# Kernel optimization log

Measured on AMD Instinct MI355X. Metric: run time of the kernel, lower is better.

Reference implementation:

```python
import jax, jax.numpy as jnp
import numpy as np

N_NODES = 50000
N_EDGES = 800000
D = 64  # in_dim = hidden_dim = out_dim


def gcn_conv(x, edge_index, W, b, num_nodes):
    """PyG GCNConv: x' = D^{-1/2} (A + I) D^{-1/2} (x W) + b."""
    h = x @ W  # [N, out]
    # add self-loops
    loop = jnp.arange(num_nodes, dtype=edge_index.dtype)
    row = jnp.concatenate([edge_index[0], loop])  # sources j
    col = jnp.concatenate([edge_index[1], loop])  # targets i
    # symmetric normalization
    ones = jnp.ones(row.shape[0], dtype=h.dtype)
    deg = jax.ops.segment_sum(ones, col, num_segments=num_nodes)
    dinv = jnp.where(deg > 0, jax.lax.rsqrt(deg), 0.0)
    norm = dinv[row] * dinv[col]  # [E+N]
    # gather -> scale -> scatter-add
    msg = h[row] * norm[:, None]
    out = jax.ops.segment_sum(msg, col, num_segments=num_nodes)
    return out + b


def setup_inputs() -> dict:
    key = jax.random.key(0)
    k = jax.random.split(key, 6)
    x = jax.random.normal(k[0], (N_NODES, D), dtype=jnp.float32)
    edge_index = jax.random.randint(k[1], (2, N_EDGES), 0, N_NODES, dtype=jnp.int64)
    s = 1.0 / np.sqrt(D)
    W1 = jax.random.uniform(k[2], (D, D), jnp.float32, -s, s)
    b1 = jnp.zeros((D,), jnp.float32)
    W2 = jax.random.uniform(k[3], (D, D), jnp.float32, -s, s)
    b2 = jnp.zeros((D,), jnp.float32)
    return {"x": x, "edge_index": edge_index, "W1": W1, "b1": b1, "W2": W2, "b2": b2}


def reference(x, edge_index, W1, b1, W2, b2):
    h = gcn_conv(x, edge_index, W1, b1, N_NODES)
    h = jax.nn.relu(h)
    out = gcn_conv(h, edge_index, W2, b2, N_NODES)
    return out
```

## Files before the change

### kernel.cpp

```cpp
#include <hip/hip_runtime.h>
#include <hip/hip_fp16.h>

#define N_NODES 50000
#define N_EDGES 800000
#define D 64
#define RANGES 8
#define SLICES 16
#define NPB (N_NODES / RANGES)
#define I4S (N_EDGES / SLICES / 4)
#define CAPS 12
#define CAP  48

__global__ __launch_bounds__(1024)
void partition_kernel(const int* __restrict__ row, const int* __restrict__ col,
                      unsigned char* __restrict__ cnt8,
                      unsigned short* __restrict__ ebuf) {
    __shared__ int cur[NPB];
    int tid = threadIdx.x;
    int r   = blockIdx.x & (RANGES - 1);
    int s   = blockIdx.x / RANGES;
    int lo  = r * NPB;
    for (int i = tid; i < NPB; i += 1024) cur[i] = 0;
    __syncthreads();
    const int4* c4 = (const int4*)col;
    const int4* r4 = (const int4*)row;
    size_t ebase = (size_t)s * N_NODES * CAPS;
    for (int i = s * I4S + tid; i < (s + 1) * I4S; i += 1024) {
        int4 c  = c4[i];
        int4 rr = r4[i];
        int dx = c.x - lo, dy = c.y - lo, dz = c.z - lo, dw = c.w - lo;
        if ((unsigned)dx < NPB) {
            int p = atomicAdd(&cur[dx], 1);
            if (p < CAPS) ebuf[ebase + (size_t)(lo + dx) * CAPS + p] = (unsigned short)rr.x;
        }
        if ((unsigned)dy < NPB) {
            int p = atomicAdd(&cur[dy], 1);
            if (p < CAPS) ebuf[ebase + (size_t)(lo + dy) * CAPS + p] = (unsigned short)rr.y;
        }
        if ((unsigned)dz < NPB) {
            int p = atomicAdd(&cur[dz], 1);
            if (p < CAPS) ebuf[ebase + (size_t)(lo + dz) * CAPS + p] = (unsigned short)rr.z;
        }
        if ((unsigned)dw < NPB) {
            int p = atomicAdd(&cur[dw], 1);
            if (p < CAPS) ebuf[ebase + (size_t)(lo + dw) * CAPS + p] = (unsigned short)rr.w;
        }
    }
    __syncthreads();
    for (int i = tid; i < NPB; i += 1024)
        cnt8[(size_t)s * N_NODES + lo + i] = (unsigned char)min(cur[i], CAPS);
}

__global__ __launch_bounds__(256)
void compact_kernel(const unsigned char* __restrict__ cnt8,
                    const unsigned short* __restrict__ ebuf,
                    unsigned short* __restrict__ srcs,
                    float* __restrict__ dinv, int* __restrict__ cntf) {
    int tid = threadIdx.x, lane = tid & 63;
    int node = blockIdx.x * 4 + (tid >> 6);
    int c = 0;
    if (lane < SLICES) c = cnt8[(size_t)lane * N_NODES + node];
    int pin = c;
    #pragma unroll
    for (int off = 1; off < SLICES; off <<= 1) {
        int t = __shfl_up(pin, off, 64);
        if (lane >= off && lane < SLICES) pin += t;
    }
    int n = __shfl(pin, SLICES - 1, 64);
    int kk = 0, pp = 0;
    #pragma unroll
    for (int k = 0; k < SLICES; ++k) {
        int Pk = __shfl(pin, k, 64);
        if (lane >= Pk) { kk = k + 1; pp = Pk; }
    }
    unsigned short v = 0;
    if (lane < n && lane < CAP)
        v = ebuf[((size_t)kk * N_NODES + node) * CAPS + (lane - pp)];
    if (lane < CAP) srcs[(size_t)node * CAP + lane] = v;
    if (lane == 0) {
        cntf[node] = min(n, CAP);
        dinv[node] = rsqrtf((float)(n + 1));
    }
}

__global__ __launch_bounds__(256)
void gemm_kernel(const float* __restrict__ X, const float* __restrict__ W,
                 __half* __restrict__ H) {
    int tid = threadIdx.x, lane = tid & 63, wv = tid >> 6;
    float w[64];
    #pragma unroll
    for (int k = 0; k < 64; ++k) w[k] = W[k * 64 + lane];
    int node0 = blockIdx.x * 16 + wv * 4;
    #pragma unroll
    for (int r = 0; r < 4; ++r) {
        int node = node0 + r;
        float xv = X[node * 64 + lane];
        float a0 = 0.f, a1 = 0.f;
        #pragma unroll
        for (int k = 0; k < 64; k += 2) {
            a0 = fmaf(__shfl(xv, k, 64),     w[k],     a0);
            a1 = fmaf(__shfl(xv, k + 1, 64), w[k + 1], a1);
        }
        H[node * 64 + lane] = __float2half(a0 + a1);
    }
}

template<int FUSE>
__global__ __launch_bounds__(256)
void gather_kernel(const __half* __restrict__ H, const int* __restrict__ cnt,
                   const unsigned short* __restrict__ srcs,
                   const float* __restrict__ dinv,
                   const float* __restrict__ bias, const float* __restrict__ W2,
                   void* __restrict__ outp) {
    int tid = threadIdx.x, lane = tid & 63;
    int node = blockIdx.x * 4 + (tid >> 6);
    int n = cnt[node];
    float di = dinv[node];
    const unsigned short* sp = srcs + (size_t)node * CAP;
    int s = 0; float w = 0.f;
    if (lane < n) { s = sp[lane]; w = dinv[s]; }
    float acc0 = di * __half2float(H[node * 64 + lane]);
    float acc1 = 0.f, acc2 = 0.f, acc3 = 0.f;
    int nr = (n + 7) & ~7;
    for (int j = 0; j < nr; j += 8) {
        int   s0 = __shfl(s, j + 0, 64), s1 = __shfl(s, j + 1, 64);
        int   s2 = __shfl(s, j + 2, 64), s3 = __shfl(s, j + 3, 64);
        int   s4 = __shfl(s, j + 4, 64), s5 = __shfl(s, j + 5, 64);
        int   s6 = __shfl(s, j + 6, 64), s7 = __shfl(s, j + 7, 64);
        float w0 = __shfl(w, j + 0, 64), w1 = __shfl(w, j + 1, 64);
        float w2 = __shfl(w, j + 2, 64), w3 = __shfl(w, j + 3, 64);
        float w4 = __shfl(w, j + 4, 64), w5 = __shfl(w, j + 5, 64);
        float w6 = __shfl(w, j + 6, 64), w7 = __shfl(w, j + 7, 64);
        float v0 = __half2float(H[s0 * 64 + lane]);
        float v1 = __half2float(H[s1 * 64 + lane]);
        float v2 = __half2float(H[s2 * 64 + lane]);
        float v3 = __half2float(H[s3 * 64 + lane]);
        float v4 = __half2float(H[s4 * 64 + lane]);
        float v5 = __half2float(H[s5 * 64 + lane]);
        float v6 = __half2float(H[s6 * 64 + lane]);
        float v7 = __half2float(H[s7 * 64 + lane]);
        acc0 += w0 * v0 + w4 * v4;
        acc1 += w1 * v1 + w5 * v5;
        acc2 += w2 * v2 + w6 * v6;
        acc3 += w3 * v3 + w7 * v7;
    }
    float gval = di * ((acc0 + acc1) + (acc2 + acc3)) + bias[lane];
    if constexpr (FUSE) {
        gval = fmaxf(gval, 0.f);
        float wc[64];
        #pragma unroll
        for (int k = 0; k < 64; ++k) wc[k] = W2[k * 64 + lane];
        float o0 = 0.f, o1 = 0.f;
        #pragma unroll
        for (int k = 0; k < 64; k += 2) {
            o0 = fmaf(__shfl(gval, k, 64),     wc[k],     o0);
            o1 = fmaf(__shfl(gval, k + 1, 64), wc[k + 1], o1);
        }
        ((__half*)outp)[node * 64 + lane] = __float2half(o0 + o1);
    } else {
        ((float*)outp)[node * 64 + lane] = gval;
    }
}

extern "C" void kernel_launch(void* const* d_in, const int* in_sizes, int n_in,
                              void* d_out, int out_size, void* d_ws, size_t ws_size,
                              hipStream_t stream) {
    const float* x   = (const float*)d_in[0];
    const int*   ei  = (const int*)d_in[1];
    const int*   row = ei;
    const int*   col = ei + N_EDGES;
    const float* W1  = (const float*)d_in[2];
    const float* b1  = (const float*)d_in[3];
    const float* W2  = (const float*)d_in[4];
    const float* b2  = (const float*)d_in[5];
    float* out = (float*)d_out;

    char* p = (char*)d_ws;
    __half* h = (__half*)p;            p += (size_t)N_NODES * D * 2;
    char* A = p;                       p += 20000000;
    unsigned short* ebuf = (unsigned short*)A;
    unsigned char*  cnt8 = (unsigned char*)(A + 19200000);
    __half* h2 = (__half*)A;
    unsigned short* srcs = (unsigned short*)p; p += (size_t)N_NODES * CAP * 2;
    float* dinv = (float*)p;           p += (size_t)N_NODES * 4;
    int*   cntf = (int*)p;             p += (size_t)N_NODES * 4;

    partition_kernel<<<RANGES * SLICES, 1024, 0, stream>>>(row, col, cnt8, ebuf);
    compact_kernel<<<N_NODES / 4, 256, 0, stream>>>(cnt8, ebuf, srcs, dinv, cntf);
    gemm_kernel<<<N_NODES / 16, 256, 0, stream>>>(x, W1, h);
    gather_kernel<1><<<N_NODES / 4, 256, 0, stream>>>(h, cntf, srcs, dinv, b1, W2, h2);
    gather_kernel<0><<<N_NODES / 4, 256, 0, stream>>>(h2, cntf, srcs, dinv, b2, nullptr, out);
}
```

Measured before the change: 225.7 us.

## Gather half2 rows with split half-waves and packed index+weight shuffles

The neighbor gather now has each half of the wavefront load half2 (two features per lane), so one wave fetches two neighbor rows per load instruction. Each source index and its fp16 normalization weight are packed into one int, which halves the shuffle count. The partial sums from the two halves are combined with an xor shuffle and then redistributed to per-feature lanes. This trades extra shuffles and the weight rounded to fp16 for fewer memory instructions and fewer shuffles per edge.

Measured after the change: 213.2 us. -5.5%, faster.

```diff
diff --git a/kernel.cpp b/kernel.cpp
--- a/kernel.cpp
+++ b/kernel.cpp
@@ -113,38 +113,60 @@
                    const float* __restrict__ bias, const float* __restrict__ W2,
                    void* __restrict__ outp) {
     int tid = threadIdx.x, lane = tid & 63;
+    int half = lane >> 5, sub = lane & 31;
     int node = blockIdx.x * 4 + (tid >> 6);
     int n = cnt[node];
     float di = dinv[node];
     const unsigned short* sp = srcs + (size_t)node * CAP;
-    int s = 0; float w = 0.f;
-    if (lane < n) { s = sp[lane]; w = dinv[s]; }
-    float acc0 = di * __half2float(H[node * 64 + lane]);
-    float acc1 = 0.f, acc2 = 0.f, acc3 = 0.f;
-    int nr = (n + 7) & ~7;
-    for (int j = 0; j < nr; j += 8) {
-        int   s0 = __shfl(s, j + 0, 64), s1 = __shfl(s, j + 1, 64);
-        int   s2 = __shfl(s, j + 2, 64), s3 = __shfl(s, j + 3, 64);
-        int   s4 = __shfl(s, j + 4, 64), s5 = __shfl(s, j + 5, 64);
-        int   s6 = __shfl(s, j + 6, 64), s7 = __shfl(s, j + 7, 64);
-        float w0 = __shfl(w, j + 0, 64), w1 = __shfl(w, j + 1, 64);
-        float w2 = __shfl(w, j + 2, 64), w3 = __shfl(w, j + 3, 64);
-        float w4 = __shfl(w, j + 4, 64), w5 = __shfl(w, j + 5, 64);
-        float w6 = __shfl(w, j + 6, 64), w7 = __shfl(w, j + 7, 64);
-        float v0 = __half2float(H[s0 * 64 + lane]);
-        float v1 = __half2float(H[s1 * 64 + lane]);
-        float v2 = __half2float(H[s2 * 64 + lane]);
-        float v3 = __half2float(H[s3 * 64 + lane]);
-        float v4 = __half2float(H[s4 * 64 + lane]);
-        float v5 = __half2float(H[s5 * 64 + lane]);
-        float v6 = __half2float(H[s6 * 64 + lane]);
-        float v7 = __half2float(H[s7 * 64 + lane]);
-        acc0 += w0 * v0 + w4 * v4;
-        acc1 += w1 * v1 + w5 * v5;
-        acc2 += w2 * v2 + w6 * v6;
-        acc3 += w3 * v3 + w7 * v7;
-    }
-    float gval = di * ((acc0 + acc1) + (acc2 + acc3)) + bias[lane];
+    int e = 0;
+    if (lane < n) {
+        int s = sp[lane];
+        float w = dinv[s];
+        e = s | (((int)__half_as_ushort(__float2half(w))) << 16);
+    }
+    const __half2* H2 = (const __half2*)H;
+    float2 self2 = __half22float2(H2[(size_t)node * 32 + sub]);
+    float sw = (half == 0) ? di : 0.f;
+    float ax = sw * self2.x, ay = sw * self2.y;
+    int i0 = half;
+    int nr = (n + 15) & ~15;
+    for (int base = 0; base < nr; base += 16) {
+        int b0 = base + i0;
+        int q0 = __shfl(e, b0 + 0,  64), q1 = __shfl(e, b0 + 2,  64);
+        int q2 = __shfl(e, b0 + 4,  64), q3 = __shfl(e, b0 + 6,  64);
+        int q4 = __shfl(e, b0 + 8,  64), q5 = __shfl(e, b0 + 10, 64);
+        int q6 = __shfl(e, b0 + 12, 64), q7 = __shfl(e, b0 + 14, 64);
+        float2 v0 = __half22float2(H2[(size_t)(q0 & 0xFFFF) * 32 + sub]);
+        float2 v1 = __half22float2(H2[(size_t)(q1 & 0xFFFF) * 32 + sub]);
+        float2 v2 = __half22float2(H2[(size_t)(q2 & 0xFFFF) * 32 + sub]);
+        float2 v3 = __half22float2(H2[(size_t)(q3 & 0xFFFF) * 32 + sub]);
+        float2 v4 = __half22float2(H2[(size_t)(q4 & 0xFFFF) * 32 + sub]);
+        float2 v5 = __half22float2(H2[(size_t)(q5 & 0xFFFF) * 32 + sub]);
+        float2 v6 = __half22float2(H2[(size_t)(q6 & 0xFFFF) * 32 + sub]);
+        float2 v7 = __half22float2(H2[(size_t)(q7 & 0xFFFF) * 32 + sub]);
+        float w0 = __half2float(__ushort_as_half((unsigned short)((unsigned)q0 >> 16)));
+        float w1 = __half2float(__ushort_as_half((unsigned short)((unsigned)q1 >> 16)));
+        float w2 = __half2float(__ushort_as_half((unsigned short)((unsigned)q2 >> 16)));
+        float w3 = __half2float(__ushort_as_half((unsigned short)((unsigned)q3 >> 16)));
+        float w4 = __half2float(__ushort_as_half((unsigned short)((unsigned)q4 >> 16)));
+        float w5 = __half2float(__ushort_as_half((unsigned short)((unsigned)q5 >> 16)));
+        float w6 = __half2float(__ushort_as_half((unsigned short)((unsigned)q6 >> 16)));
+        float w7 = __half2float(__ushort_as_half((unsigned short)((unsigned)q7 >> 16)));
+        ax = fmaf(w0, v0.x, ax); ay = fmaf(w0, v0.y, ay);
+        ax = fmaf(w1, v1.x, ax); ay = fmaf(w1, v1.y, ay);
+        ax = fmaf(w2, v2.x, ax); ay = fmaf(w2, v2.y, ay);
+        ax = fmaf(w3, v3.x, ax); ay = fmaf(w3, v3.y, ay);
+        ax = fmaf(w4, v4.x, ax); ay = fmaf(w4, v4.y, ay);
+        ax = fmaf(w5, v5.x, ax); ay = fmaf(w5, v5.y, ay);
+        ax = fmaf(w6, v6.x, ax); ay = fmaf(w6, v6.y, ay);
+        ax = fmaf(w7, v7.x, ax); ay = fmaf(w7, v7.y, ay);
+    }
+    ax += __shfl_xor(ax, 32, 64);
+    ay += __shfl_xor(ay, 32, 64);
+    float cx = __shfl(ax, lane >> 1, 64);
+    float cy = __shfl(ay, lane >> 1, 64);
+    float sum = (lane & 1) ? cy : cx;
+    float gval = di * sum + bias[lane];
     if constexpr (FUSE) {
         gval = fmaxf(gval, 0.f);
         float wc[64];
```
